# Kernel optimization log

Hardware: AMD Instinct MI355X
Metric: run time of the kernel (lower is better)

Reference implementation:

```python
import jax, jax.numpy as jnp
import numpy as np

MARGIN = 0.3


def setup_inputs() -> dict:
    key = jax.random.key(0)
    k1, k2 = jax.random.split(key)
    inputs = jax.random.normal(k1, (8192, 256), dtype=jnp.float32)
    targets = jax.random.randint(k2, (8192,), 0, 512, dtype=jnp.int64)
    return {"inputs": inputs, "targets": targets}


def reference(inputs, targets):
    # L2-normalize features (normalize_feature=True default)
    x = inputs / (jnp.linalg.norm(inputs, axis=-1, keepdims=True) + 1e-12)
    n = x.shape[0]
    # pairwise euclidean distance [n, n]
    sq = jnp.sum(x * x, axis=1)
    dist = sq[:, None] + sq[None, :] - 2.0 * (x @ x.T)
    dist = jnp.sqrt(jnp.clip(dist, 1e-12, None))
    # positive / negative masks
    same = targets[:, None] == targets[None, :]
    eye = jnp.eye(n, dtype=bool)
    is_same = same & ~eye          # positives, diagonal excluded
    is_diff = ~same                # negatives
    neg_inf = jnp.float32(-jnp.inf)
    pos_inf = jnp.float32(jnp.inf)
    # hard positive: max over positives per row (fallback 0.0 if none)
    dist_ap = jnp.max(jnp.where(is_same, dist, neg_inf), axis=1)
    dist_ap = jnp.where(jnp.any(is_same, axis=1), dist_ap, 0.0)
    # hard negative: min over negatives per row (fallback margin+1 if none)
    dist_an = jnp.min(jnp.where(is_diff, dist, pos_inf), axis=1)
    dist_an = jnp.where(jnp.any(is_diff, axis=1), dist_an, MARGIN + 1.0)
    # MarginRankingLoss with y=1: mean(max(0, -(an - ap) + margin))
    loss = jnp.mean(jnp.maximum(0.0, dist_ap - dist_an + MARGIN))
    return loss
```

## Files before the change

kernel.cpp:

```cpp
#include <hip/hip_runtime.h>
#include <hip/hip_bf16.h>

#define NROWS  8192
#define DIM    256
#define NCLASS 512
#define MARGIN 0.3f

using bf16x8 = __attribute__((ext_vector_type(8))) short;
using f32x4  = __attribute__((ext_vector_type(4))) float;

__device__ inline ushort f2bf(float f) {
    __hip_bfloat16 h = __float2bfloat16(f);
    return *reinterpret_cast<ushort*>(&h);
}
__device__ inline float bf2f(ushort u) {
    return __uint_as_float(((unsigned)u) << 16);
}
__device__ inline unsigned f2ord(float f) {
    unsigned b = __float_as_uint(f);
    return (b & 0x80000000u) ? ~b : (b | 0x80000000u);
}
__device__ inline float ord2f(unsigned u) {
    return __uint_as_float((u & 0x80000000u) ? (u & 0x7FFFFFFFu) : ~u);
}
__device__ inline void ld16_g2l(const void* g, void* l) {
    __builtin_amdgcn_global_load_lds(
        (const __attribute__((address_space(1))) unsigned int*)g,
        (__attribute__((address_space(3))) unsigned int*)l, 16, 0, 0);
}

#define XBS_OFF 0u
#define SQS_OFF 4194304u
#define TGT_OFF 4227072u
#define PMX_OFF 4259840u
#define NMN_OFF 4292608u
#define BIN_OFF 4325376u
#define ACC_OFF 4327424u
#define TIK_OFF 4327432u

__global__ __launch_bounds__(512) void hist_scan_kernel(
    const int* __restrict__ tgt, int* __restrict__ bincur,
    double* __restrict__ accd, unsigned* __restrict__ ticket)
{
    __shared__ int h[NCLASS];
    int tid = threadIdx.x;
    h[tid] = 0;
    if (tid == 0) { *accd = 0.0; *ticket = 0u; }
    __syncthreads();
    for (int k = 0; k < NROWS / NCLASS; ++k)
        atomicAdd(&h[tgt[tid + k * NCLASS]], 1);
    __syncthreads();
    int cnt = h[tid];
    for (int ofs = 1; ofs < NCLASS; ofs <<= 1) {
        int v = (tid >= ofs) ? h[tid - ofs] : 0;
        __syncthreads();
        h[tid] += v;
        __syncthreads();
    }
    bincur[tid] = h[tid] - cnt;
}

__global__ __launch_bounds__(256) void norm_scatter_kernel(
    const float* __restrict__ in, const int* __restrict__ tgt,
    int* __restrict__ bincur, ushort* __restrict__ xbs,
    float* __restrict__ sqs, int* __restrict__ tgts,
    unsigned* __restrict__ pmax, unsigned* __restrict__ nmin)
{
    int row  = blockIdx.x * 4 + (threadIdx.x >> 6);
    int lane = threadIdx.x & 63;
    float4 v = ((const float4*)(in + (size_t)row * DIM))[lane];
    float ss = v.x * v.x + v.y * v.y + v.z * v.z + v.w * v.w;
#pragma unroll
    for (int m = 1; m < 64; m <<= 1) ss += __shfl_xor(ss, m, 64);
    float inv = 1.0f / (sqrtf(ss) + 1e-12f);

    ushort4 st;
    st.x = f2bf(v.x * inv); st.y = f2bf(v.y * inv);
    st.z = f2bf(v.z * inv); st.w = f2bf(v.w * inv);

    int t = 0, dst = 0;
    if (lane == 0) { t = tgt[row]; dst = atomicAdd(&bincur[t], 1); }
    dst = __shfl(dst, 0); t = __shfl(t, 0);

    ((ushort4*)(xbs + (size_t)dst * DIM))[lane] = st;

    float a0 = bf2f(st.x), a1 = bf2f(st.y), a2 = bf2f(st.z), a3 = bf2f(st.w);
    float s2 = a0 * a0 + a1 * a1 + a2 * a2 + a3 * a3;
#pragma unroll
    for (int m = 1; m < 64; m <<= 1) s2 += __shfl_xor(s2, m, 64);
    if (lane == 0) {
        sqs[dst]  = s2;
        tgts[dst] = t;
        pmax[dst] = 0x007FFFFFu;
        nmin[dst] = 0xFF800000u;
    }
}

__global__ __launch_bounds__(256, 2) void gram_kernel(
    const ushort* __restrict__ xbs, const float* __restrict__ sqs,
    const int* __restrict__ tgts, unsigned* __restrict__ pmax,
    unsigned* __restrict__ nmin)
{
    __shared__ struct {
        char  buf[2][16384];
        float sqc[512];
        int   tgc[512];
        int   tga[256];
    } sm;

    const int wave = threadIdx.x >> 6;
    const int lane = threadIdx.x & 63;
    const int l15  = lane & 15;
    const int quad = lane >> 4;
    const int mbase = blockIdx.x * 256 + wave * 64;
    const int nbase = blockIdx.y * 512;

    {
        int c = threadIdx.x * 2;
        sm.sqc[c]     = sqs[nbase + c];
        sm.sqc[c + 1] = sqs[nbase + c + 1];
        sm.tgc[c]     = tgts[nbase + c];
        sm.tgc[c + 1] = tgts[nbase + c + 1];
        sm.tga[threadIdx.x] = tgts[blockIdx.x * 256 + threadIdx.x];
    }

    bf16x8 afrag[4][8];
#pragma unroll
    for (int a = 0; a < 4; ++a) {
        const ushort* arow = xbs + (size_t)(mbase + a * 16 + l15) * DIM + quad * 8;
#pragma unroll
        for (int kk = 0; kk < 8; ++kk)
            afrag[a][kk] = *(const bf16x8*)(arow + kk * 32);
    }
    const int rlo = tgts[mbase];
    const int rhi = tgts[mbase + 63];

    const int colh = lane >> 5, c31 = lane & 31;
    int offs[4];
#pragma unroll
    for (int j = 0; j < 4; ++j)
        offs[j] = colh * 512 + ((c31 ^ ((2 * j + colh) & 7)) << 4);

    const char* xbs_b = (const char*)xbs;

    {
        const char* gbase = xbs_b + (size_t)nbase * 512;
#pragma unroll
        for (int j = 0; j < 4; ++j) {
            int i = wave * 4 + j;
            ld16_g2l(gbase + i * 1024 + offs[j], sm.buf[0] + i * 1024);
        }
    }
    __syncthreads();

    float pm[16], nm[16];
#pragma unroll
    for (int j = 0; j < 16; ++j) { pm[j] = -__builtin_inff(); nm[j] = __builtin_inff(); }

#pragma unroll 2
    for (int s = 0; s < 16; ++s) {
        if (s < 15) {
            const char* gbase = xbs_b + (size_t)(nbase + (s + 1) * 32) * 512;
            char* lbase = sm.buf[(s + 1) & 1];
#pragma unroll
            for (int j = 0; j < 4; ++j) {
                int i = wave * 4 + j;
                ld16_g2l(gbase + i * 1024 + offs[j], lbase + i * 1024);
            }
        }
        const char* bufc = sm.buf[s & 1];
#pragma unroll
        for (int u = 0; u < 2; ++u) {
            const int t16 = s * 32 + u * 16;
            bf16x8 bfrag[8];
#pragma unroll
            for (int kk = 0; kk < 8; ++kk)
                bfrag[kk] = *(const bf16x8*)(bufc + u * 8192 + l15 * 512 +
                                             (((quad + 4 * kk) ^ (l15 & 7)) << 4));
            f32x4 acc4[4];
#pragma unroll
            for (int a = 0; a < 4; ++a) {
                f32x4 acc = {0.f, 0.f, 0.f, 0.f};
#pragma unroll
                for (int kk = 0; kk < 8; ++kk)
                    acc = __builtin_amdgcn_mfma_f32_16x16x32_bf16(afrag[a][kk], bfrag[kk], acc, 0, 0, 0);
                acc4[a] = acc;
            }
            const float sqc = sm.sqc[t16 + l15];
            const int clo = sm.tgc[t16], chi = sm.tgc[t16 + 15];
            if (rlo <= chi && clo <= rhi) {
                const int tc = sm.tgc[t16 + l15];
#pragma unroll
                for (int a = 0; a < 4; ++a)
#pragma unroll
                    for (int i = 0; i < 4; ++i) {
                        const float v = fmaf(acc4[a][i], -2.0f, sqc);
                        const bool same = (sm.tga[wave * 64 + a * 16 + quad * 4 + i] == tc);
                        pm[a * 4 + i] = fmaxf(pm[a * 4 + i], same ? v : -__builtin_inff());
                        nm[a * 4 + i] = fminf(nm[a * 4 + i], same ? __builtin_inff() : v);
                    }
            } else {
#pragma unroll
                for (int a = 0; a < 4; ++a)
#pragma unroll
                    for (int i = 0; i < 4; ++i)
                        nm[a * 4 + i] = fminf(nm[a * 4 + i], fmaf(acc4[a][i], -2.0f, sqc));
            }
        }
        __syncthreads();
    }

#pragma unroll
    for (int m = 1; m < 16; m <<= 1) {
#pragma unroll
        for (int j = 0; j < 16; ++j) {
            pm[j] = fmaxf(pm[j], __shfl_xor(pm[j], m, 64));
            nm[j] = fminf(nm[j], __shfl_xor(nm[j], m, 64));
        }
    }
    if (l15 == 0) {
#pragma unroll
        for (int a = 0; a < 4; ++a)
#pragma unroll
            for (int i = 0; i < 4; ++i) {
                int r = mbase + a * 16 + quad * 4 + i;
                atomicMax(&pmax[r], f2ord(pm[a * 4 + i]));
                atomicMin(&nmin[r], f2ord(nm[a * 4 + i]));
            }
    }
}

__global__ __launch_bounds__(256) void finalize_kernel(
    const unsigned* __restrict__ pmax, const unsigned* __restrict__ nmin,
    const float* __restrict__ sqs, double* __restrict__ accd,
    unsigned* __restrict__ ticket, float* __restrict__ out)
{
    int r = blockIdx.x * 256 + threadIdx.x;
    float pe = ord2f(pmax[r]);
    float ne = ord2f(nmin[r]);
    float ap = sqrtf(fmaxf(sqs[r] + pe, 0.0f));
    float an = (ne > 1e30f) ? (MARGIN + 1.0f) : sqrtf(fmaxf(sqs[r] + ne, 0.0f));
    float h  = fmaxf(ap - an + MARGIN, 0.0f);
    double s = (double)h;
#pragma unroll
    for (int m = 1; m < 64; m <<= 1) s += __shfl_xor(s, m, 64);
    __shared__ double sh[4];
    if ((threadIdx.x & 63) == 0) sh[threadIdx.x >> 6] = s;
    __syncthreads();
    if (threadIdx.x == 0) {
        double b = sh[0] + sh[1] + sh[2] + sh[3];
        atomicAdd(accd, b);
        __threadfence();
        unsigned old = atomicAdd(ticket, 1u);
        if (old == gridDim.x - 1) {
            double total = atomicAdd(accd, 0.0);
            out[0] = (float)(total / (double)NROWS);
        }
    }
}

extern "C" void kernel_launch(void* const* d_in, const int* in_sizes, int n_in,
                              void* d_out, int out_size, void* d_ws, size_t ws_size,
                              hipStream_t stream) {
    const float* in  = (const float*)d_in[0];
    const int*   tgt = (const int*)d_in[1];
    float*       out = (float*)d_out;

    char* ws = (char*)d_ws;
    ushort*   xbs    = (ushort*)(ws + XBS_OFF);
    float*    sqs    = (float*)(ws + SQS_OFF);
    int*      tgts   = (int*)(ws + TGT_OFF);
    unsigned* pmax   = (unsigned*)(ws + PMX_OFF);
    unsigned* nmin   = (unsigned*)(ws + NMN_OFF);
    int*      bincur = (int*)(ws + BIN_OFF);
    double*   accd   = (double*)(ws + ACC_OFF);
    unsigned* ticket = (unsigned*)(ws + TIK_OFF);

    hist_scan_kernel<<<1, 512, 0, stream>>>(tgt, bincur, accd, ticket);
    norm_scatter_kernel<<<NROWS / 4, 256, 0, stream>>>(in, tgt, bincur, xbs, sqs, tgts, pmax, nmin);
    gram_kernel<<<dim3(32, 16), 256, 0, stream>>>(xbs, sqs, tgts, pmax, nmin);
    finalize_kernel<<<32, 256, 0, stream>>>(pmax, nmin, sqs, accd, ticket, out);
}
```

Baseline: 114.9 us.

## Load B fragments directly from global into registers with XCD-aware block swizzle

Drops the LDS double buffer filled by global_load_lds and the per-stage block barriers in the Gram kernel. Each wave now loads its B fragments straight from global memory into registers, double-buffered across 16-column tiles, and raises wave priority around the MFMA bursts. The grid becomes 1D with an XCD-aware remap so that blocks on the same XCD share A and B tiles in L2. The trade-off is that each wave fetches B data separately instead of sharing it through LDS, which raises global/L2 traffic and register pressure.

```diff
diff --git a/kernel.cpp b/kernel.cpp
--- a/kernel.cpp
+++ b/kernel.cpp
@@ -22,11 +22,6 @@
 }
 __device__ inline float ord2f(unsigned u) {
     return __uint_as_float((u & 0x80000000u) ? (u & 0x7FFFFFFFu) : ~u);
-}
-__device__ inline void ld16_g2l(const void* g, void* l) {
-    __builtin_amdgcn_global_load_lds(
-        (const __attribute__((address_space(1))) unsigned int*)g,
-        (__attribute__((address_space(3))) unsigned int*)l, 16, 0, 0);
 }
 
 #define XBS_OFF 0u
@@ -102,7 +97,6 @@
     unsigned* __restrict__ nmin)
 {
     __shared__ struct {
-        char  buf[2][16384];
         float sqc[512];
         int   tgc[512];
         int   tga[256];
@@ -112,8 +106,15 @@
     const int lane = threadIdx.x & 63;
     const int l15  = lane & 15;
     const int quad = lane >> 4;
-    const int mbase = blockIdx.x * 256 + wave * 64;
-    const int nbase = blockIdx.y * 512;
+
+    const int id  = blockIdx.x;
+    const int xcd = id & 7;
+    const int w   = id >> 3;
+    const int bx  = (xcd & 3) * 8 + (w & 7);
+    const int by  = (xcd >> 2) * 8 + (w >> 3);
+
+    const int mbase = bx * 256 + wave * 64;
+    const int nbase = by * 512;
 
     {
         int c = threadIdx.x * 2;
@@ -121,7 +122,7 @@
         sm.sqc[c + 1] = sqs[nbase + c + 1];
         sm.tgc[c]     = tgts[nbase + c];
         sm.tgc[c + 1] = tgts[nbase + c + 1];
-        sm.tga[threadIdx.x] = tgts[blockIdx.x * 256 + threadIdx.x];
+        sm.tga[threadIdx.x] = tgts[bx * 256 + threadIdx.x];
     }
 
     bf16x8 afrag[4][8];
@@ -135,80 +136,74 @@
     const int rlo = tgts[mbase];
     const int rhi = tgts[mbase + 63];
 
-    const int colh = lane >> 5, c31 = lane & 31;
-    int offs[4];
-#pragma unroll
-    for (int j = 0; j < 4; ++j)
-        offs[j] = colh * 512 + ((c31 ^ ((2 * j + colh) & 7)) << 4);
-
-    const char* xbs_b = (const char*)xbs;
-
-    {
-        const char* gbase = xbs_b + (size_t)nbase * 512;
-#pragma unroll
-        for (int j = 0; j < 4; ++j) {
-            int i = wave * 4 + j;
-            ld16_g2l(gbase + i * 1024 + offs[j], sm.buf[0] + i * 1024);
-        }
-    }
     __syncthreads();
 
     float pm[16], nm[16];
 #pragma unroll
     for (int j = 0; j < 16; ++j) { pm[j] = -__builtin_inff(); nm[j] = __builtin_inff(); }
 
-#pragma unroll 2
-    for (int s = 0; s < 16; ++s) {
-        if (s < 15) {
-            const char* gbase = xbs_b + (size_t)(nbase + (s + 1) * 32) * 512;
-            char* lbase = sm.buf[(s + 1) & 1];
-#pragma unroll
-            for (int j = 0; j < 4; ++j) {
-                int i = wave * 4 + j;
-                ld16_g2l(gbase + i * 1024 + offs[j], lbase + i * 1024);
-            }
-        }
-        const char* bufc = sm.buf[s & 1];
-#pragma unroll
-        for (int u = 0; u < 2; ++u) {
-            const int t16 = s * 32 + u * 16;
-            bf16x8 bfrag[8];
-#pragma unroll
-            for (int kk = 0; kk < 8; ++kk)
-                bfrag[kk] = *(const bf16x8*)(bufc + u * 8192 + l15 * 512 +
-                                             (((quad + 4 * kk) ^ (l15 & 7)) << 4));
-            f32x4 acc4[4];
-#pragma unroll
-            for (int a = 0; a < 4; ++a) {
-                f32x4 acc = {0.f, 0.f, 0.f, 0.f};
-#pragma unroll
-                for (int kk = 0; kk < 8; ++kk)
-                    acc = __builtin_amdgcn_mfma_f32_16x16x32_bf16(afrag[a][kk], bfrag[kk], acc, 0, 0, 0);
-                acc4[a] = acc;
-            }
-            const float sqc = sm.sqc[t16 + l15];
-            const int clo = sm.tgc[t16], chi = sm.tgc[t16 + 15];
-            if (rlo <= chi && clo <= rhi) {
-                const int tc = sm.tgc[t16 + l15];
-#pragma unroll
-                for (int a = 0; a < 4; ++a)
-#pragma unroll
-                    for (int i = 0; i < 4; ++i) {
-                        const float v = fmaf(acc4[a][i], -2.0f, sqc);
-                        const bool same = (sm.tga[wave * 64 + a * 16 + quad * 4 + i] == tc);
-                        pm[a * 4 + i] = fmaxf(pm[a * 4 + i], same ? v : -__builtin_inff());
-                        nm[a * 4 + i] = fminf(nm[a * 4 + i], same ? __builtin_inff() : v);
-                    }
-            } else {
-#pragma unroll
-                for (int a = 0; a < 4; ++a)
-#pragma unroll
-                    for (int i = 0; i < 4; ++i)
-                        nm[a * 4 + i] = fminf(nm[a * 4 + i], fmaf(acc4[a][i], -2.0f, sqc));
-            }
-        }
-        __syncthreads();
-    }
+    const ushort* bbase = xbs + (size_t)nbase * DIM + quad * 8;
+
+    bf16x8 bfA[8], bfB[8];
+
+#define LOADB_H(buf, t, h) do {                                              \
+        const ushort* p_ = bbase + (size_t)((t) * 16 + l15) * DIM;           \
+        _Pragma("unroll")                                                    \
+        for (int kk = 4 * (h); kk < 4 * (h) + 4; ++kk)                       \
+            buf[kk] = *(const bf16x8*)(p_ + kk * 32);                        \
+    } while (0)
+
+#define TILE(t, buf, pt, pbuf) do {                                          \
+        const int   t16_ = (t) * 16;                                         \
+        const float sqc_ = sm.sqc[t16_ + l15];                               \
+        const int   clo_ = sm.tgc[t16_], chi_ = sm.tgc[t16_ + 15];           \
+        const int   tc_  = sm.tgc[t16_ + l15];                               \
+        const bool  slow_ = (rlo <= chi_ && clo_ <= rhi);                    \
+        _Pragma("unroll")                                                    \
+        for (int h = 0; h < 2; ++h) {                                        \
+            f32x4 acc0_ = {0.f, 0.f, 0.f, 0.f};                              \
+            f32x4 acc1_ = {0.f, 0.f, 0.f, 0.f};                              \
+            if ((pt) >= 0) LOADB_H(pbuf, pt, h);     \
+            __builtin_amdgcn_s_setprio(1);                                   \
+            _Pragma("unroll")                                                \
+            for (int kk = 0; kk < 8; ++kk) {                                 \
+                acc0_ = __builtin_amdgcn_mfma_f32_16x16x32_bf16(             \
+                            afrag[2 * h][kk],     buf[kk], acc0_, 0, 0, 0);  \
+                acc1_ = __builtin_amdgcn_mfma_f32_16x16x32_bf16(             \
+                            afrag[2 * h + 1][kk], buf[kk], acc1_, 0, 0, 0);  \
+            }                                                                \
+            __builtin_amdgcn_s_setprio(0);                                   \
+            if (slow_) {                                                     \
+                _Pragma("unroll")                                            \
+                for (int i = 0; i < 4; ++i) {                                \
+                    const float v0_ = fmaf(acc0_[i], -2.0f, sqc_);           \
+                    const bool  s0_ = (sm.tga[wave * 64 + (2 * h) * 16 + quad * 4 + i] == tc_); \
+                    pm[(2 * h) * 4 + i] = fmaxf(pm[(2 * h) * 4 + i], s0_ ? v0_ : -__builtin_inff()); \
+                    nm[(2 * h) * 4 + i] = fminf(nm[(2 * h) * 4 + i], s0_ ? __builtin_inff() : v0_);  \
+                    const float v1_ = fmaf(acc1_[i], -2.0f, sqc_);           \
+                    const bool  s1_ = (sm.tga[wave * 64 + (2 * h + 1) * 16 + quad * 4 + i] == tc_); \
+                    pm[(2 * h + 1) * 4 + i] = fmaxf(pm[(2 * h + 1) * 4 + i], s1_ ? v1_ : -__builtin_inff()); \
+                    nm[(2 * h + 1) * 4 + i] = fminf(nm[(2 * h + 1) * 4 + i], s1_ ? __builtin_inff() : v1_);  \
+                }                                                            \
+            } else {                                                         \
+                _Pragma("unroll")                                            \
+                for (int i = 0; i < 4; ++i) {                                \
+                    nm[(2 * h) * 4 + i]     = fminf(nm[(2 * h) * 4 + i],     fmaf(acc0_[i], -2.0f, sqc_)); \
+                    nm[(2 * h + 1) * 4 + i] = fminf(nm[(2 * h + 1) * 4 + i], fmaf(acc1_[i], -2.0f, sqc_)); \
+                }                                                            \
+            }                                                                \
+        }                                                                    \
+    } while (0)
+
+    LOADB_H(bfA, 0, 0);
+    LOADB_H(bfA, 0, 1);
+#pragma unroll 1
+    for (int t = 0; t < 32; t += 2) {
+        TILE(t, bfA, t + 1, bfB);
+        TILE(t + 1, bfB, (t + 2 < 32) ? (t + 2) : -1, bfA);
+    }
+#undef LOADB_H
+#undef TILE
 
 #pragma unroll
     for (int m = 1; m < 16; m <<= 1) {
@@ -278,6 +273,6 @@
 
     hist_scan_kernel<<<1, 512, 0, stream>>>(tgt, bincur, accd, ticket);
     norm_scatter_kernel<<<NROWS / 4, 256, 0, stream>>>(in, tgt, bincur, xbs, sqs, tgts, pmax, nmin);
-    gram_kernel<<<dim3(32, 16), 256, 0, stream>>>(xbs, sqs, tgts, pmax, nmin);
+    gram_kernel<<<512, 256, 0, stream>>>(xbs, sqs, tgts, pmax, nmin);
     finalize_kernel<<<32, 256, 0, stream>>>(pmax, nmin, sqs, accd, ticket, out);
 }
```

New measurement: 166.7 us. 45.1% more time.

## Shrink gram tiles, remap blocks per XCD, and fuse finalize into last block

Applied to the files above, without the earlier changes.

Halves the row tile per wave (32 rows instead of 64) and launches 1024 blocks instead of 512, with an XCD-aware block-index remap so blocks on the same XCD share row and column panels in L2. It raises the occupancy hint to three blocks per CU, keeps row targets in registers, and turns off unrolling of the main loop. The separate finalize kernel is folded into the gram kernel through a last-block ticket, which saves one launch. In exchange, each block reloads the B panel for half as many rows, and the final reduction now runs serially in a single block.

```diff
diff --git a/kernel.cpp b/kernel.cpp
--- a/kernel.cpp
+++ b/kernel.cpp
@@ -35,17 +35,16 @@
 #define PMX_OFF 4259840u
 #define NMN_OFF 4292608u
 #define BIN_OFF 4325376u
-#define ACC_OFF 4327424u
-#define TIK_OFF 4327432u
+#define TIK_OFF 4327424u
 
 __global__ __launch_bounds__(512) void hist_scan_kernel(
     const int* __restrict__ tgt, int* __restrict__ bincur,
-    double* __restrict__ accd, unsigned* __restrict__ ticket)
+    unsigned* __restrict__ ticket)
 {
     __shared__ int h[NCLASS];
     int tid = threadIdx.x;
     h[tid] = 0;
-    if (tid == 0) { *accd = 0.0; *ticket = 0u; }
+    if (tid == 0) *ticket = 0u;
     __syncthreads();
     for (int k = 0; k < NROWS / NCLASS; ++k)
         atomicAdd(&h[tgt[tid + k * NCLASS]], 1);
@@ -96,24 +95,33 @@
     }
 }
 
-__global__ __launch_bounds__(256, 2) void gram_kernel(
+__global__ __launch_bounds__(256, 3) void gram_kernel(
     const ushort* __restrict__ xbs, const float* __restrict__ sqs,
     const int* __restrict__ tgts, unsigned* __restrict__ pmax,
-    unsigned* __restrict__ nmin)
+    unsigned* __restrict__ nmin, unsigned* __restrict__ ticket,
+    float* __restrict__ out)
 {
     __shared__ struct {
         char  buf[2][16384];
         float sqc[512];
         int   tgc[512];
-        int   tga[256];
+        int   tga[128];
     } sm;
+    __shared__ unsigned lastblk;
 
     const int wave = threadIdx.x >> 6;
     const int lane = threadIdx.x & 63;
     const int l15  = lane & 15;
     const int quad = lane >> 4;
-    const int mbase = blockIdx.x * 256 + wave * 64;
-    const int nbase = blockIdx.y * 512;
+
+    const int id  = blockIdx.x;
+    const int xcd = id & 7;
+    const int w   = id >> 3;
+    const int bx  = (xcd & 3) * 16 + (w & 15);
+    const int by  = (xcd >> 2) * 8 + (w >> 4);
+
+    const int wbase = bx * 128 + wave * 32;
+    const int nbase = by * 512;
 
     {
         int c = threadIdx.x * 2;
@@ -121,19 +129,26 @@
         sm.sqc[c + 1] = sqs[nbase + c + 1];
         sm.tgc[c]     = tgts[nbase + c];
         sm.tgc[c + 1] = tgts[nbase + c + 1];
-        sm.tga[threadIdx.x] = tgts[blockIdx.x * 256 + threadIdx.x];
-    }
-
-    bf16x8 afrag[4][8];
-#pragma unroll
-    for (int a = 0; a < 4; ++a) {
-        const ushort* arow = xbs + (size_t)(mbase + a * 16 + l15) * DIM + quad * 8;
+        if (threadIdx.x < 128)
+            sm.tga[threadIdx.x] = tgts[bx * 128 + threadIdx.x];
+    }
+
+    bf16x8 afrag[2][8];
+#pragma unroll
+    for (int a = 0; a < 2; ++a) {
+        const ushort* arow = xbs + (size_t)(wbase + a * 16 + l15) * DIM + quad * 8;
 #pragma unroll
         for (int kk = 0; kk < 8; ++kk)
             afrag[a][kk] = *(const bf16x8*)(arow + kk * 32);
     }
-    const int rlo = tgts[mbase];
-    const int rhi = tgts[mbase + 63];
+    const int rlo = tgts[wbase];
+    const int rhi = tgts[wbase + 31];
+    int tgr[8];
+#pragma unroll
+    for (int a = 0; a < 2; ++a)
+#pragma unroll
+        for (int i = 0; i < 4; ++i)
+            tgr[a * 4 + i] = tgts[wbase + a * 16 + quad * 4 + i];
 
     const int colh = lane >> 5, c31 = lane & 31;
     int offs[4];
@@ -153,11 +168,11 @@
     }
     __syncthreads();
 
-    float pm[16], nm[16];
-#pragma unroll
-    for (int j = 0; j < 16; ++j) { pm[j] = -__builtin_inff(); nm[j] = __builtin_inff(); }
-
-#pragma unroll 2
+    float pm[8], nm[8];
+#pragma unroll
+    for (int j = 0; j < 8; ++j) { pm[j] = -__builtin_inff(); nm[j] = __builtin_inff(); }
+
+#pragma unroll 1
     for (int s = 0; s < 16; ++s) {
         if (s < 15) {
             const char* gbase = xbs_b + (size_t)(nbase + (s + 1) * 32) * 512;
@@ -177,9 +192,9 @@
             for (int kk = 0; kk < 8; ++kk)
                 bfrag[kk] = *(const bf16x8*)(bufc + u * 8192 + l15 * 512 +
                                              (((quad + 4 * kk) ^ (l15 & 7)) << 4));
-            f32x4 acc4[4];
-#pragma unroll
-            for (int a = 0; a < 4; ++a) {
+            f32x4 acc4[2];
+#pragma unroll
+            for (int a = 0; a < 2; ++a) {
                 f32x4 acc = {0.f, 0.f, 0.f, 0.f};
 #pragma unroll
                 for (int kk = 0; kk < 8; ++kk)
@@ -191,17 +206,17 @@
             if (rlo <= chi && clo <= rhi) {
                 const int tc = sm.tgc[t16 + l15];
 #pragma unroll
-                for (int a = 0; a < 4; ++a)
+                for (int a = 0; a < 2; ++a)
 #pragma unroll
                     for (int i = 0; i < 4; ++i) {
                         const float v = fmaf(acc4[a][i], -2.0f, sqc);
-                        const bool same = (sm.tga[wave * 64 + a * 16 + quad * 4 + i] == tc);
+                        const bool same = (tgr[a * 4 + i] == tc);
                         pm[a * 4 + i] = fmaxf(pm[a * 4 + i], same ? v : -__builtin_inff());
                         nm[a * 4 + i] = fminf(nm[a * 4 + i], same ? __builtin_inff() : v);
                     }
             } else {
 #pragma unroll
-                for (int a = 0; a < 4; ++a)
+                for (int a = 0; a < 2; ++a)
 #pragma unroll
                     for (int i = 0; i < 4; ++i)
                         nm[a * 4 + i] = fminf(nm[a * 4 + i], fmaf(acc4[a][i], -2.0f, sqc));
@@ -213,49 +228,47 @@
 #pragma unroll
     for (int m = 1; m < 16; m <<= 1) {
 #pragma unroll
-        for (int j = 0; j < 16; ++j) {
+        for (int j = 0; j < 8; ++j) {
             pm[j] = fmaxf(pm[j], __shfl_xor(pm[j], m, 64));
             nm[j] = fminf(nm[j], __shfl_xor(nm[j], m, 64));
         }
     }
     if (l15 == 0) {
 #pragma unroll
-        for (int a = 0; a < 4; ++a)
+        for (int a = 0; a < 2; ++a)
 #pragma unroll
             for (int i = 0; i < 4; ++i) {
-                int r = mbase + a * 16 + quad * 4 + i;
+                int r = wbase + a * 16 + quad * 4 + i;
                 atomicMax(&pmax[r], f2ord(pm[a * 4 + i]));
                 atomicMin(&nmin[r], f2ord(nm[a * 4 + i]));
             }
     }
-}
-
-__global__ __launch_bounds__(256) void finalize_kernel(
-    const unsigned* __restrict__ pmax, const unsigned* __restrict__ nmin,
-    const float* __restrict__ sqs, double* __restrict__ accd,
-    unsigned* __restrict__ ticket, float* __restrict__ out)
-{
-    int r = blockIdx.x * 256 + threadIdx.x;
-    float pe = ord2f(pmax[r]);
-    float ne = ord2f(nmin[r]);
-    float ap = sqrtf(fmaxf(sqs[r] + pe, 0.0f));
-    float an = (ne > 1e30f) ? (MARGIN + 1.0f) : sqrtf(fmaxf(sqs[r] + ne, 0.0f));
-    float h  = fmaxf(ap - an + MARGIN, 0.0f);
-    double s = (double)h;
-#pragma unroll
-    for (int m = 1; m < 64; m <<= 1) s += __shfl_xor(s, m, 64);
-    __shared__ double sh[4];
-    if ((threadIdx.x & 63) == 0) sh[threadIdx.x >> 6] = s;
-    __syncthreads();
-    if (threadIdx.x == 0) {
-        double b = sh[0] + sh[1] + sh[2] + sh[3];
-        atomicAdd(accd, b);
+
+    __threadfence();
+    if (threadIdx.x == 0)
+        lastblk = (atomicAdd(ticket, 1u) == 1023u) ? 1u : 0u;
+    __syncthreads();
+    if (lastblk) {
         __threadfence();
-        unsigned old = atomicAdd(ticket, 1u);
-        if (old == gridDim.x - 1) {
-            double total = atomicAdd(accd, 0.0);
-            out[0] = (float)(total / (double)NROWS);
-        }
+        double s = 0.0;
+        for (int r = threadIdx.x; r < NROWS; r += 256) {
+            unsigned pu = __hip_atomic_load(&pmax[r], __ATOMIC_RELAXED,
+                                            __HIP_MEMORY_SCOPE_AGENT);
+            unsigned nu = __hip_atomic_load(&nmin[r], __ATOMIC_RELAXED,
+                                            __HIP_MEMORY_SCOPE_AGENT);
+            float pe = ord2f(pu);
+            float ne = ord2f(nu);
+            float ap = sqrtf(fmaxf(sqs[r] + pe, 0.0f));
+            float an = (ne > 1e30f) ? (MARGIN + 1.0f) : sqrtf(fmaxf(sqs[r] + ne, 0.0f));
+            s += (double)fmaxf(ap - an + MARGIN, 0.0f);
+        }
+#pragma unroll
+        for (int m = 1; m < 64; m <<= 1) s += __shfl_xor(s, m, 64);
+        __shared__ double sh[4];
+        if ((threadIdx.x & 63) == 0) sh[threadIdx.x >> 6] = s;
+        __syncthreads();
+        if (threadIdx.x == 0)
+            out[0] = (float)((sh[0] + sh[1] + sh[2] + sh[3]) / (double)NROWS);
     }
 }
 
@@ -273,11 +286,9 @@
     unsigned* pmax   = (unsigned*)(ws + PMX_OFF);
     unsigned* nmin   = (unsigned*)(ws + NMN_OFF);
     int*      bincur = (int*)(ws + BIN_OFF);
-    double*   accd   = (double*)(ws + ACC_OFF);
     unsigned* ticket = (unsigned*)(ws + TIK_OFF);
 
-    hist_scan_kernel<<<1, 512, 0, stream>>>(tgt, bincur, accd, ticket);
+    hist_scan_kernel<<<1, 512, 0, stream>>>(tgt, bincur, ticket);
     norm_scatter_kernel<<<NROWS / 4, 256, 0, stream>>>(in, tgt, bincur, xbs, sqs, tgts, pmax, nmin);
-    gram_kernel<<<dim3(32, 16), 256, 0, stream>>>(xbs, sqs, tgts, pmax, nmin);
-    finalize_kernel<<<32, 256, 0, stream>>>(pmax, nmin, sqs, accd, ticket, out);
-}
+    gram_kernel<<<1024, 256, 0, stream>>>(xbs, sqs, tgts, pmax, nmin, ticket, out);
+}
```

Measured after the change: 191.2 us. +66.4%, slower.

## Fuse histogram into prep kernel with grid barrier; fold finalize into gram

Applied to the files above, without the earlier changes.

Merges the single-block histogram/scan kernel and the normalize-scatter kernel into one 512-block prep kernel. It builds the class histogram with global atomics, syncs through a software grid barrier, then has every block redo the prefix scan locally. The finalize kernel is removed: the last gram block, picked by an atomic ticket, computes the loss reduction. This cuts kernel launches and serial single-block work, but adds a memset, a spin barrier that assumes all 512 blocks are co-resident, and a serial final reduction in one block.

```diff
diff --git a/kernel.cpp b/kernel.cpp
--- a/kernel.cpp
+++ b/kernel.cpp
@@ -34,72 +34,89 @@
 #define TGT_OFF 4227072u
 #define PMX_OFF 4259840u
 #define NMN_OFF 4292608u
-#define BIN_OFF 4325376u
-#define ACC_OFF 4327424u
-#define TIK_OFF 4327432u
-
-__global__ __launch_bounds__(512) void hist_scan_kernel(
-    const int* __restrict__ tgt, int* __restrict__ bincur,
-    double* __restrict__ accd, unsigned* __restrict__ ticket)
-{
-    __shared__ int h[NCLASS];
-    int tid = threadIdx.x;
-    h[tid] = 0;
-    if (tid == 0) { *accd = 0.0; *ticket = 0u; }
-    __syncthreads();
-    for (int k = 0; k < NROWS / NCLASS; ++k)
-        atomicAdd(&h[tgt[tid + k * NCLASS]], 1);
-    __syncthreads();
-    int cnt = h[tid];
-    for (int ofs = 1; ofs < NCLASS; ofs <<= 1) {
-        int v = (tid >= ofs) ? h[tid - ofs] : 0;
-        __syncthreads();
-        h[tid] += v;
-        __syncthreads();
-    }
-    bincur[tid] = h[tid] - cnt;
-}
-
-__global__ __launch_bounds__(256) void norm_scatter_kernel(
+#define HST_OFF 4325376u
+#define CNT_OFF 4327424u
+#define TIK_OFF 4329472u
+#define BAR_OFF 4329476u
+
+#define PREP_BLOCKS 512
+
+__global__ __launch_bounds__(256) void prep_kernel(
     const float* __restrict__ in, const int* __restrict__ tgt,
-    int* __restrict__ bincur, ushort* __restrict__ xbs,
-    float* __restrict__ sqs, int* __restrict__ tgts,
+    int* __restrict__ hist, int* __restrict__ cnt2, unsigned* __restrict__ bar,
+    ushort* __restrict__ xbs, float* __restrict__ sqs, int* __restrict__ tgts,
     unsigned* __restrict__ pmax, unsigned* __restrict__ nmin)
 {
-    int row  = blockIdx.x * 4 + (threadIdx.x >> 6);
-    int lane = threadIdx.x & 63;
-    float4 v = ((const float4*)(in + (size_t)row * DIM))[lane];
-    float ss = v.x * v.x + v.y * v.y + v.z * v.z + v.w * v.w;
-#pragma unroll
-    for (int m = 1; m < 64; m <<= 1) ss += __shfl_xor(ss, m, 64);
-    float inv = 1.0f / (sqrtf(ss) + 1e-12f);
-
-    ushort4 st;
-    st.x = f2bf(v.x * inv); st.y = f2bf(v.y * inv);
-    st.z = f2bf(v.z * inv); st.w = f2bf(v.w * inv);
-
-    int t = 0, dst = 0;
-    if (lane == 0) { t = tgt[row]; dst = atomicAdd(&bincur[t], 1); }
-    dst = __shfl(dst, 0); t = __shfl(t, 0);
-
-    ((ushort4*)(xbs + (size_t)dst * DIM))[lane] = st;
-
-    float a0 = bf2f(st.x), a1 = bf2f(st.y), a2 = bf2f(st.z), a3 = bf2f(st.w);
-    float s2 = a0 * a0 + a1 * a1 + a2 * a2 + a3 * a3;
-#pragma unroll
-    for (int m = 1; m < 64; m <<= 1) s2 += __shfl_xor(s2, m, 64);
-    if (lane == 0) {
-        sqs[dst]  = s2;
-        tgts[dst] = t;
-        pmax[dst] = 0x007FFFFFu;
-        nmin[dst] = 0xFF800000u;
+    const int b   = blockIdx.x;
+    const int tid = threadIdx.x;
+
+    if (tid < 16) atomicAdd(&hist[tgt[b * 16 + tid]], 1);
+
+    __threadfence();
+    __syncthreads();
+    if (tid == 0) {
+        __hip_atomic_fetch_add(bar, 1u, __ATOMIC_ACQ_REL, __HIP_MEMORY_SCOPE_AGENT);
+        while (__hip_atomic_load(bar, __ATOMIC_ACQUIRE, __HIP_MEMORY_SCOPE_AGENT)
+               < (unsigned)PREP_BLOCKS)
+            __builtin_amdgcn_s_sleep(2);
+    }
+    __syncthreads();
+
+    __shared__ int h[NCLASS];
+    h[tid]       = hist[tid];
+    h[tid + 256] = hist[tid + 256];
+    __syncthreads();
+    for (int ofs = 1; ofs < NCLASS; ofs <<= 1) {
+        int v0 = (tid >= ofs) ? h[tid - ofs] : 0;
+        int v1 = (tid + 256 >= ofs) ? h[tid + 256 - ofs] : 0;
+        __syncthreads();
+        h[tid]       += v0;
+        h[tid + 256] += v1;
+        __syncthreads();
+    }
+
+    const int wv   = tid >> 6;
+    const int lane = tid & 63;
+#pragma unroll 1
+    for (int rr = 0; rr < 4; ++rr) {
+        int row = b * 16 + wv * 4 + rr;
+        float4 v = ((const float4*)(in + (size_t)row * DIM))[lane];
+        float ss = v.x * v.x + v.y * v.y + v.z * v.z + v.w * v.w;
+#pragma unroll
+        for (int m = 1; m < 64; m <<= 1) ss += __shfl_xor(ss, m, 64);
+        float inv = 1.0f / (sqrtf(ss) + 1e-12f);
+
+        ushort4 st;
+        st.x = f2bf(v.x * inv); st.y = f2bf(v.y * inv);
+        st.z = f2bf(v.z * inv); st.w = f2bf(v.w * inv);
+
+        int t = 0, dst = 0;
+        if (lane == 0) {
+            t = tgt[row];
+            dst = (h[t] - hist[t]) + atomicAdd(&cnt2[t], 1);
+        }
+        dst = __shfl(dst, 0); t = __shfl(t, 0);
+
+        ((ushort4*)(xbs + (size_t)dst * DIM))[lane] = st;
+
+        float a0 = bf2f(st.x), a1 = bf2f(st.y), a2 = bf2f(st.z), a3 = bf2f(st.w);
+        float s2 = a0 * a0 + a1 * a1 + a2 * a2 + a3 * a3;
+#pragma unroll
+        for (int m = 1; m < 64; m <<= 1) s2 += __shfl_xor(s2, m, 64);
+        if (lane == 0) {
+            sqs[dst]  = s2;
+            tgts[dst] = t;
+            pmax[dst] = 0x007FFFFFu;
+            nmin[dst] = 0xFF800000u;
+        }
     }
 }
 
 __global__ __launch_bounds__(256, 2) void gram_kernel(
     const ushort* __restrict__ xbs, const float* __restrict__ sqs,
     const int* __restrict__ tgts, unsigned* __restrict__ pmax,
-    unsigned* __restrict__ nmin)
+    unsigned* __restrict__ nmin, unsigned* __restrict__ ticket,
+    float* __restrict__ out)
 {
     __shared__ struct {
         char  buf[2][16384];
@@ -107,6 +124,7 @@
         int   tgc[512];
         int   tga[256];
     } sm;
+    __shared__ unsigned lastblk;
 
     const int wave = threadIdx.x >> 6;
     const int lane = threadIdx.x & 63;
@@ -228,34 +246,32 @@
                 atomicMin(&nmin[r], f2ord(nm[a * 4 + i]));
             }
     }
-}
-
-__global__ __launch_bounds__(256) void finalize_kernel(
-    const unsigned* __restrict__ pmax, const unsigned* __restrict__ nmin,
-    const float* __restrict__ sqs, double* __restrict__ accd,
-    unsigned* __restrict__ ticket, float* __restrict__ out)
-{
-    int r = blockIdx.x * 256 + threadIdx.x;
-    float pe = ord2f(pmax[r]);
-    float ne = ord2f(nmin[r]);
-    float ap = sqrtf(fmaxf(sqs[r] + pe, 0.0f));
-    float an = (ne > 1e30f) ? (MARGIN + 1.0f) : sqrtf(fmaxf(sqs[r] + ne, 0.0f));
-    float h  = fmaxf(ap - an + MARGIN, 0.0f);
-    double s = (double)h;
-#pragma unroll
-    for (int m = 1; m < 64; m <<= 1) s += __shfl_xor(s, m, 64);
-    __shared__ double sh[4];
-    if ((threadIdx.x & 63) == 0) sh[threadIdx.x >> 6] = s;
-    __syncthreads();
-    if (threadIdx.x == 0) {
-        double b = sh[0] + sh[1] + sh[2] + sh[3];
-        atomicAdd(accd, b);
+
+    __threadfence();
+    if (threadIdx.x == 0)
+        lastblk = (atomicAdd(ticket, 1u) == 511u) ? 1u : 0u;
+    __syncthreads();
+    if (lastblk) {
         __threadfence();
-        unsigned old = atomicAdd(ticket, 1u);
-        if (old == gridDim.x - 1) {
-            double total = atomicAdd(accd, 0.0);
-            out[0] = (float)(total / (double)NROWS);
-        }
+        double s = 0.0;
+        for (int r = threadIdx.x; r < NROWS; r += 256) {
+            unsigned pu = __hip_atomic_load(&pmax[r], __ATOMIC_RELAXED,
+                                            __HIP_MEMORY_SCOPE_AGENT);
+            unsigned nu = __hip_atomic_load(&nmin[r], __ATOMIC_RELAXED,
+                                            __HIP_MEMORY_SCOPE_AGENT);
+            float pe = ord2f(pu);
+            float ne = ord2f(nu);
+            float ap = sqrtf(fmaxf(sqs[r] + pe, 0.0f));
+            float an = (ne > 1e30f) ? (MARGIN + 1.0f) : sqrtf(fmaxf(sqs[r] + ne, 0.0f));
+            s += (double)fmaxf(ap - an + MARGIN, 0.0f);
+        }
+#pragma unroll
+        for (int m = 1; m < 64; m <<= 1) s += __shfl_xor(s, m, 64);
+        __shared__ double sh[4];
+        if ((threadIdx.x & 63) == 0) sh[threadIdx.x >> 6] = s;
+        __syncthreads();
+        if (threadIdx.x == 0)
+            out[0] = (float)((sh[0] + sh[1] + sh[2] + sh[3]) / (double)NROWS);
     }
 }
 
@@ -272,12 +288,14 @@
     int*      tgts   = (int*)(ws + TGT_OFF);
     unsigned* pmax   = (unsigned*)(ws + PMX_OFF);
     unsigned* nmin   = (unsigned*)(ws + NMN_OFF);
-    int*      bincur = (int*)(ws + BIN_OFF);
-    double*   accd   = (double*)(ws + ACC_OFF);
+    int*      hist   = (int*)(ws + HST_OFF);
+    int*      cnt2   = (int*)(ws + CNT_OFF);
     unsigned* ticket = (unsigned*)(ws + TIK_OFF);
-
-    hist_scan_kernel<<<1, 512, 0, stream>>>(tgt, bincur, accd, ticket);
-    norm_scatter_kernel<<<NROWS / 4, 256, 0, stream>>>(in, tgt, bincur, xbs, sqs, tgts, pmax, nmin);
-    gram_kernel<<<dim3(32, 16), 256, 0, stream>>>(xbs, sqs, tgts, pmax, nmin);
-    finalize_kernel<<<32, 256, 0, stream>>>(pmax, nmin, sqs, accd, ticket, out);
-}
+    unsigned* bar    = (unsigned*)(ws + BAR_OFF);
+
+    hipMemsetAsync(ws + HST_OFF, 0, 4104, stream);
+    prep_kernel<<<PREP_BLOCKS, 256, 0, stream>>>(in, tgt, hist, cnt2, bar,
+                                                 xbs, sqs, tgts, pmax, nmin);
+    gram_kernel<<<dim3(32, 16), 256, 0, stream>>>(xbs, sqs, tgts, pmax, nmin,
+                                                  ticket, out);
+}
```

Result: slower. 191.3 us (+66.5%).
